# Kernel optimization log

Measured on AMD Instinct MI355X. Metric: run time of the kernel, lower is better.

The kernel has to match this reference:

```python
import jax, jax.numpy as jnp
from jax import lax
import numpy as np

D = 4      # agent_state_vector_length
H = 32     # hidden width (hardcoded in module)
N = 128    # agents
T = 100    # timesteps


def setup_inputs() -> dict:
    key = jax.random.key(0)
    ks = jax.random.split(key, 16)
    g = lambda k, s: jax.random.normal(k, s, dtype=jnp.float32) * 0.05
    return {
        "x": jax.random.normal(ks[0], (N, T, D), dtype=jnp.float32),
        # Conv1d weights stored [out_ch, in_ch, k] (OIH)
        "w1": g(ks[1], (16, D, 3)), "b1": g(ks[2], (16,)),
        "w2": g(ks[3], (32, 16, 3)), "b2": g(ks[4], (32,)),
        "w3": g(ks[5], (32, 32, 3)), "b3": g(ks[6], (32,)),
        # Linear weights stored [in, out]
        "We": g(ks[7], (2 * H, H)), "be": g(ks[8], (H,)),
        "Wa": g(ks[9], (H, H)),     "ba": g(ks[10], (H,)),
        "Wu": g(ks[11], (2 * H, H)), "bu": g(ks[12], (H,)),
        "Wd": g(ks[13], (H, D)),    "bd": g(ks[14], (D,)),
    }


def _forward(x, w1, b1, w2, b2, w3, b3, We, be, Wa, ba, Wu, bu, Wd, bd):
    # ---- conv_1d: per-agent temporal encoder (agents batched) ----
    h = jnp.transpose(x, (0, 2, 1))  # [N, D, T]
    def conv(h, w, b):
        y = lax.conv_general_dilated(h, w, (1,), 'VALID',
                                     dimension_numbers=('NCH', 'OIH', 'NCH'))
        return jax.nn.relu(y + b[None, :, None])
    h = conv(h, w1, b1)
    h = conv(h, w2, b2)
    h = conv(h, w3, b3)            # [N, H, T-6]
    h = jnp.transpose(h, (2, 0, 1))  # [T', N, H]  (time_steps)
    Tp = h.shape[0]

    # ---- graph_conv: all-pairs edge MLP + sum aggregation (j != i) ----
    Wj, Wi = We[:H], We[H:]          # concat(node_j, node_i) split
    ej = jnp.einsum('tjc,cd->tjd', h, Wj)  # sender part
    ei = jnp.einsum('tic,cd->tid', h, Wi)  # receiver part
    e = jax.nn.relu(ej[:, None, :, :] + ei[:, :, None, :] + be)  # [T',i,j,H]
    diag = jax.nn.relu(ej + ei + be)       # i == j terms, excluded by loop
    agg = e.sum(axis=2) - diag             # [T', N, H]
    agg = jax.nn.relu(agg @ Wa + ba)
    upd = jax.nn.relu(h @ Wu[:H] + agg @ Wu[H:] + bu)  # concat(node_i, agg)

    # ---- decode: residual over original state at t+6 ----
    dec = upd @ Wd + bd                    # [T', N, D]
    out = x[:, 6:6 + Tp] + jnp.transpose(dec, (1, 0, 2))  # [N, T', D]
    return out


def reference(x, w1, b1, w2, b2, w3, b3, We, be, Wa, ba, Wu, bu, Wd, bd):
    return _forward(x, w1, b1, w2, b2, w3, b3, We, be, Wa, ba, Wu, bu, Wd, bd)
```

## Files before the change

kernel.cpp:

```cpp
#include <hip/hip_runtime.h>


#define NN 128
#define TT 100
#define TP 94
#define HH 32

__global__ __launch_bounds__(256) void k_conv(
    const float* __restrict__ x,
    const float* __restrict__ w1, const float* __restrict__ b1,
    const float* __restrict__ w2, const float* __restrict__ b2,
    const float* __restrict__ w3, const float* __restrict__ b3,
    const float* __restrict__ We,
    float* __restrict__ h_g, float* __restrict__ ej_g, float* __restrict__ ei_g)
{
    __shared__ float sx[4][72];
    __shared__ float s1[16][68];
    __shared__ float s2[32][64];
    __shared__ float s3[32][48];

    const int n    = blockIdx.x;
    const int half = blockIdx.y;
    const int t0g  = half * 46;
    const int tid  = threadIdx.x;

    if (tid < 72) {
        float4 v = make_float4(0.f, 0.f, 0.f, 0.f);
        if (tid < 54) v = ((const float4*)x)[n * TT + t0g + tid];
        sx[0][tid] = v.x; sx[1][tid] = v.y; sx[2][tid] = v.z; sx[3][tid] = v.w;
    }
    __syncthreads();

    for (int idx = tid; idx < 16 * 68; idx += 256) {
        int o = idx / 68, t = idx - o * 68;
        float acc = b1[o];
        #pragma unroll
        for (int i = 0; i < 4; ++i)
            #pragma unroll
            for (int k = 0; k < 3; ++k)
                acc += sx[i][t + k] * w1[o * 12 + i * 3 + k];
        s1[o][t] = fmaxf(acc, 0.f);
    }
    __syncthreads();

    {
        const int o = tid & 31, seg = tid >> 5;
        const int t0 = seg * 8;
        float acc[8];
        float bv = b2[o];
        #pragma unroll
        for (int u = 0; u < 8; ++u) acc[u] = bv;
        #pragma unroll
        for (int i = 0; i < 16; ++i) {
            float4 f0 = *(const float4*)&s1[i][t0];
            float4 f1 = *(const float4*)&s1[i][t0 + 4];
            float4 f2 = *(const float4*)&s1[i][t0 + 8];
            float a[12] = {f0.x, f0.y, f0.z, f0.w, f1.x, f1.y, f1.z, f1.w,
                           f2.x, f2.y, f2.z, f2.w};
            float W0 = w2[o * 48 + i * 3 + 0];
            float W1 = w2[o * 48 + i * 3 + 1];
            float W2 = w2[o * 48 + i * 3 + 2];
            #pragma unroll
            for (int u = 0; u < 8; ++u)
                acc[u] += a[u] * W0 + a[u + 1] * W1 + a[u + 2] * W2;
        }
        #pragma unroll
        for (int u = 0; u < 8; ++u) s2[o][t0 + u] = fmaxf(acc[u], 0.f);
    }
    __syncthreads();

    {
        const int o = tid & 31, seg = tid >> 5;
        if (seg < 6) {
            const int t0 = seg * 8;
            float acc[8];
            float bv = b3[o];
            #pragma unroll
            for (int u = 0; u < 8; ++u) acc[u] = bv;
            #pragma unroll
            for (int i = 0; i < 32; ++i) {
                float4 f0 = *(const float4*)&s2[i][t0];
                float4 f1 = *(const float4*)&s2[i][t0 + 4];
                float4 f2 = *(const float4*)&s2[i][t0 + 8];
                float a[12] = {f0.x, f0.y, f0.z, f0.w, f1.x, f1.y, f1.z, f1.w,
                               f2.x, f2.y, f2.z, f2.w};
                float W0 = w3[o * 96 + i * 3 + 0];
                float W1 = w3[o * 96 + i * 3 + 1];
                float W2 = w3[o * 96 + i * 3 + 2];
                #pragma unroll
                for (int u = 0; u < 8; ++u)
                    acc[u] += a[u] * W0 + a[u + 1] * W1 + a[u + 2] * W2;
            }
            #pragma unroll
            for (int u = 0; u < 8; ++u) s3[o][t0 + u] = fmaxf(acc[u], 0.f);
        }
    }
    __syncthreads();

    for (int idx = tid; idx < 48 * 32; idx += 256) {
        int tl = idx >> 5, o = idx & 31;
        h_g[((t0g + tl) * NN + n) * HH + o] = s3[o][tl];
    }

    {
        const int d = tid & 31, seg = tid >> 5;
        if (seg < 6) {
            const int t0 = seg * 8;
            float aj[8], ai[8];
            #pragma unroll
            for (int u = 0; u < 8; ++u) { aj[u] = 0.f; ai[u] = 0.f; }
            #pragma unroll
            for (int c = 0; c < 32; ++c) {
                float4 f0 = *(const float4*)&s3[c][t0];
                float4 f1 = *(const float4*)&s3[c][t0 + 4];
                float hv[8] = {f0.x, f0.y, f0.z, f0.w, f1.x, f1.y, f1.z, f1.w};
                float wj = We[c * 32 + d];
                float wi = We[(32 + c) * 32 + d];
                #pragma unroll
                for (int u = 0; u < 8; ++u) {
                    aj[u] += hv[u] * wj;
                    ai[u] += hv[u] * wi;
                }
            }
            #pragma unroll
            for (int u = 0; u < 8; ++u) {
                int tg = t0g + t0 + u;
                ej_g[(tg * NN + n) * HH + d] = aj[u];
                ei_g[(tg * NN + n) * HH + d] = ai[u];
            }
        }
    }
}

__global__ __launch_bounds__(256) void k_agg(
    const float* __restrict__ x,
    const float* __restrict__ h_g, const float* __restrict__ ej_g,
    const float* __restrict__ ei_g,
    const float* __restrict__ be, const float* __restrict__ Wa,
    const float* __restrict__ ba, const float* __restrict__ Wu,
    const float* __restrict__ bu, const float* __restrict__ Wd,
    const float* __restrict__ bd, float* __restrict__ out)
{
    const int t  = blockIdx.x;
    const int ib = blockIdx.y;
    const int tid = threadIdx.x;

    __shared__ float sej[NN * HH];
    __shared__ float sei[32 * HH];
    __shared__ float sh[32 * HH];
    __shared__ float sagg[32 * HH];
    __shared__ float sagg2[32 * HH];
    __shared__ float supd[32 * HH];

    {
        const float4* ej4 = (const float4*)(ej_g + t * NN * HH);
        float4* s4 = (float4*)sej;
        #pragma unroll
        for (int u = 0; u < 4; ++u) s4[tid + 256 * u] = ej4[tid + 256 * u];
        const float4* ei4 = (const float4*)(ei_g + (t * NN + ib * 32) * HH);
        const float4* h4  = (const float4*)(h_g  + (t * NN + ib * 32) * HH);
        ((float4*)sei)[tid] = ei4[tid];
        ((float4*)sh)[tid]  = h4[tid];
    }
    __syncthreads();

    const int d  = tid & 31;
    const int i0 = tid >> 5;

    {
        float bev = be[d];
        float c[4], acc[4];
        #pragma unroll
        for (int u = 0; u < 4; ++u) {
            int i = i0 + u * 8;
            c[u] = sei[i * HH + d] + bev;
            acc[u] = -fmaxf(sej[(ib * 32 + i) * HH + d] + c[u], 0.f);
        }
        #pragma unroll 8
        for (int j = 0; j < NN; ++j) {
            float v = sej[j * HH + d];
            #pragma unroll
            for (int u = 0; u < 4; ++u)
                acc[u] += fmaxf(v + c[u], 0.f);
        }
        #pragma unroll
        for (int u = 0; u < 4; ++u)
            sagg[(i0 + u * 8) * HH + d] = acc[u];
    }
    __syncthreads();

    {
        float acc[4];
        float bav = ba[d];
        #pragma unroll
        for (int u = 0; u < 4; ++u) acc[u] = bav;
        #pragma unroll
        for (int c = 0; c < 32; ++c) {
            float wa = Wa[c * 32 + d];
            #pragma unroll
            for (int u = 0; u < 4; ++u)
                acc[u] += sagg[(i0 + u * 8) * HH + c] * wa;
        }
        #pragma unroll
        for (int u = 0; u < 4; ++u)
            sagg2[(i0 + u * 8) * HH + d] = fmaxf(acc[u], 0.f);
    }
    __syncthreads();

    {
        float acc[4];
        float buv = bu[d];
        #pragma unroll
        for (int u = 0; u < 4; ++u) acc[u] = buv;
        #pragma unroll
        for (int c = 0; c < 32; ++c) {
            float wh = Wu[c * 32 + d];
            float wg = Wu[(32 + c) * 32 + d];
            #pragma unroll
            for (int u = 0; u < 4; ++u) {
                int i = i0 + u * 8;
                acc[u] += sh[i * HH + c] * wh + sagg2[i * HH + c] * wg;
            }
        }
        #pragma unroll
        for (int u = 0; u < 4; ++u)
            supd[(i0 + u * 8) * HH + d] = fmaxf(acc[u], 0.f);
    }
    __syncthreads();

    if (tid < 128) {
        int i = tid >> 2, d4 = tid & 3;
        int n = ib * 32 + i;
        float a = bd[d4];
        #pragma unroll
        for (int c = 0; c < 32; ++c)
            a += supd[i * HH + c] * Wd[c * 4 + d4];
        out[n * (TP * 4) + t * 4 + d4] = x[n * (TT * 4) + (6 + t) * 4 + d4] + a;
    }
}

extern "C" void kernel_launch(void* const* d_in, const int* in_sizes, int n_in,
                              void* d_out, int out_size, void* d_ws, size_t ws_size,
                              hipStream_t stream) {
    const float* x  = (const float*)d_in[0];
    const float* w1 = (const float*)d_in[1];
    const float* b1 = (const float*)d_in[2];
    const float* w2 = (const float*)d_in[3];
    const float* b2 = (const float*)d_in[4];
    const float* w3 = (const float*)d_in[5];
    const float* b3 = (const float*)d_in[6];
    const float* We = (const float*)d_in[7];
    const float* be = (const float*)d_in[8];
    const float* Wa = (const float*)d_in[9];
    const float* ba = (const float*)d_in[10];
    const float* Wu = (const float*)d_in[11];
    const float* bu = (const float*)d_in[12];
    const float* Wd = (const float*)d_in[13];
    const float* bd = (const float*)d_in[14];

    float* ws   = (float*)d_ws;
    float* h_g  = ws;
    float* ej_g = ws + TP * NN * HH;
    float* ei_g = ws + 2 * TP * NN * HH;

    k_conv<<<dim3(NN, 2), 256, 0, stream>>>(x, w1, b1, w2, b2, w3, b3, We,
                                            h_g, ej_g, ei_g);
    k_agg<<<dim3(TP, 4), 256, 0, stream>>>(x, h_g, ej_g, ei_g,
                                           be, Wa, ba, Wu, bu, Wd, bd,
                                           (float*)d_out);
}
```

Measured before the change: 102.8 us.

## Fuse conv and graph-aggregation kernels into one cooperative kernel with grid sync

Merges the two kernel launches into a single cooperative kernel of 384 blocks. The first phase computes the conv stack plus the ej/ei projections on time-thirds, and the second phase runs the per-timestep aggregation, separated by a grid-wide sync. Shared memory for the two phases is overlaid through a union, and the conv stage is re-tiled so each thread computes two output channels. This removes one launch and the inter-kernel gap, at the cost of grid-sync overhead and a cooperative-launch residency requirement.

```diff
diff --git a/kernel.cpp b/kernel.cpp
--- a/kernel.cpp
+++ b/kernel.cpp
@@ -1,4 +1,7 @@
 #include <hip/hip_runtime.h>
+#include <hip/hip_cooperative_groups.h>
+
+namespace cg = cooperative_groups;
 
 
 #define NN 128
@@ -6,236 +9,264 @@
 #define TP 94
 #define HH 32
 
-__global__ __launch_bounds__(256) void k_conv(
+union SharedU {
+    struct {
+        float sx[4][40];
+        float s1[16][44];
+        float s2[32][40];
+        float s3[32][32];
+    } a;
+    struct {
+        float sej[NN * HH];
+        float sei[32 * HH];
+        float sh[32 * HH];
+        float sagg[32 * HH];
+        float sagg2[32 * HH];
+        float supd[32 * HH];
+    } b;
+};
+
+__global__ __launch_bounds__(256, 2) void k_fused(
     const float* __restrict__ x,
     const float* __restrict__ w1, const float* __restrict__ b1,
     const float* __restrict__ w2, const float* __restrict__ b2,
     const float* __restrict__ w3, const float* __restrict__ b3,
-    const float* __restrict__ We,
-    float* __restrict__ h_g, float* __restrict__ ej_g, float* __restrict__ ei_g)
+    const float* __restrict__ We, const float* __restrict__ be,
+    const float* __restrict__ Wa, const float* __restrict__ ba,
+    const float* __restrict__ Wu, const float* __restrict__ bu,
+    const float* __restrict__ Wd, const float* __restrict__ bd,
+    float* __restrict__ h_g, float* __restrict__ ej_g,
+    float* __restrict__ ei_g, float* __restrict__ out)
 {
-    __shared__ float sx[4][72];
-    __shared__ float s1[16][68];
-    __shared__ float s2[32][64];
-    __shared__ float s3[32][48];
-
-    const int n    = blockIdx.x;
-    const int half = blockIdx.y;
-    const int t0g  = half * 46;
-    const int tid  = threadIdx.x;
-
-    if (tid < 72) {
-        float4 v = make_float4(0.f, 0.f, 0.f, 0.f);
-        if (tid < 54) v = ((const float4*)x)[n * TT + t0g + tid];
-        sx[0][tid] = v.x; sx[1][tid] = v.y; sx[2][tid] = v.z; sx[3][tid] = v.w;
+    __shared__ SharedU S;
+    const int tid = threadIdx.x;
+
+    {
+        const int bid   = blockIdx.x;
+        const int n     = bid / 3;
+        const int third = bid - n * 3;
+        const int t0g   = third * 31;
+
+        if (tid < 38) {
+            float4 v = ((const float4*)x)[n * TT + t0g + tid];
+            S.a.sx[0][tid] = v.x; S.a.sx[1][tid] = v.y;
+            S.a.sx[2][tid] = v.z; S.a.sx[3][tid] = v.w;
+        }
+        __syncthreads();
+
+        for (int idx = tid; idx < 16 * 36; idx += 256) {
+            int o = idx / 36, t = idx - o * 36;
+            float acc = b1[o];
+            #pragma unroll
+            for (int i = 0; i < 4; ++i)
+                #pragma unroll
+                for (int k = 0; k < 3; ++k)
+                    acc += S.a.sx[i][t + k] * w1[o * 12 + i * 3 + k];
+            S.a.s1[o][t] = fmaxf(acc, 0.f);
+        }
+        __syncthreads();
+
+        {
+            const int o = tid & 15, seg = tid >> 4;
+            if (seg < 5) {
+                const int t0 = seg * 8;
+                float acc0[8], acc1[8];
+                float bv0 = b2[o], bv1 = b2[o + 16];
+                #pragma unroll
+                for (int u = 0; u < 8; ++u) { acc0[u] = bv0; acc1[u] = bv1; }
+                #pragma unroll
+                for (int i = 0; i < 16; ++i) {
+                    float4 f0 = *(const float4*)&S.a.s1[i][t0];
+                    float4 f1 = *(const float4*)&S.a.s1[i][t0 + 4];
+                    float4 f2 = *(const float4*)&S.a.s1[i][t0 + 8];
+                    float a[12] = {f0.x, f0.y, f0.z, f0.w, f1.x, f1.y, f1.z,
+                                   f1.w, f2.x, f2.y, f2.z, f2.w};
+                    float W00 = w2[o * 48 + i * 3 + 0];
+                    float W01 = w2[o * 48 + i * 3 + 1];
+                    float W02 = w2[o * 48 + i * 3 + 2];
+                    float W10 = w2[(o + 16) * 48 + i * 3 + 0];
+                    float W11 = w2[(o + 16) * 48 + i * 3 + 1];
+                    float W12 = w2[(o + 16) * 48 + i * 3 + 2];
+                    #pragma unroll
+                    for (int u = 0; u < 8; ++u) {
+                        acc0[u] += a[u] * W00 + a[u + 1] * W01 + a[u + 2] * W02;
+                        acc1[u] += a[u] * W10 + a[u + 1] * W11 + a[u + 2] * W12;
+                    }
+                }
+                #pragma unroll
+                for (int u = 0; u < 8; ++u) {
+                    S.a.s2[o][t0 + u]      = fmaxf(acc0[u], 0.f);
+                    S.a.s2[o + 16][t0 + u] = fmaxf(acc1[u], 0.f);
+                }
+            }
+        }
+        __syncthreads();
+
+        {
+            const int o = tid & 15, seg = tid >> 4;
+            if (seg < 4) {
+                const int t0 = seg * 8;
+                float acc0[8], acc1[8];
+                float bv0 = b3[o], bv1 = b3[o + 16];
+                #pragma unroll
+                for (int u = 0; u < 8; ++u) { acc0[u] = bv0; acc1[u] = bv1; }
+                #pragma unroll
+                for (int i = 0; i < 32; ++i) {
+                    float4 f0 = *(const float4*)&S.a.s2[i][t0];
+                    float4 f1 = *(const float4*)&S.a.s2[i][t0 + 4];
+                    float4 f2 = *(const float4*)&S.a.s2[i][t0 + 8];
+                    float a[12] = {f0.x, f0.y, f0.z, f0.w, f1.x, f1.y, f1.z,
+                                   f1.w, f2.x, f2.y, f2.z, f2.w};
+                    float W00 = w3[o * 96 + i * 3 + 0];
+                    float W01 = w3[o * 96 + i * 3 + 1];
+                    float W02 = w3[o * 96 + i * 3 + 2];
+                    float W10 = w3[(o + 16) * 96 + i * 3 + 0];
+                    float W11 = w3[(o + 16) * 96 + i * 3 + 1];
+                    float W12 = w3[(o + 16) * 96 + i * 3 + 2];
+                    #pragma unroll
+                    for (int u = 0; u < 8; ++u) {
+                        acc0[u] += a[u] * W00 + a[u + 1] * W01 + a[u + 2] * W02;
+                        acc1[u] += a[u] * W10 + a[u + 1] * W11 + a[u + 2] * W12;
+                    }
+                }
+                #pragma unroll
+                for (int u = 0; u < 8; ++u) {
+                    S.a.s3[o][t0 + u]      = fmaxf(acc0[u], 0.f);
+                    S.a.s3[o + 16][t0 + u] = fmaxf(acc1[u], 0.f);
+                }
+            }
+        }
+        __syncthreads();
+
+        for (int idx = tid; idx < 32 * 32; idx += 256) {
+            int tl = idx >> 5, o = idx & 31;
+            h_g[((t0g + tl) * NN + n) * HH + o] = S.a.s3[o][tl];
+        }
+
+        {
+            const int d = tid & 31, seg = tid >> 5;
+            if (seg < 4) {
+                const int t0 = seg * 8;
+                float aj[8], ai[8];
+                #pragma unroll
+                for (int u = 0; u < 8; ++u) { aj[u] = 0.f; ai[u] = 0.f; }
+                #pragma unroll
+                for (int c = 0; c < 32; ++c) {
+                    float4 f0 = *(const float4*)&S.a.s3[c][t0];
+                    float4 f1 = *(const float4*)&S.a.s3[c][t0 + 4];
+                    float hv[8] = {f0.x, f0.y, f0.z, f0.w, f1.x, f1.y, f1.z, f1.w};
+                    float wj = We[c * 32 + d];
+                    float wi = We[(32 + c) * 32 + d];
+                    #pragma unroll
+                    for (int u = 0; u < 8; ++u) {
+                        aj[u] += hv[u] * wj;
+                        ai[u] += hv[u] * wi;
+                    }
+                }
+                #pragma unroll
+                for (int u = 0; u < 8; ++u) {
+                    int tg = t0g + t0 + u;
+                    ej_g[(tg * NN + n) * HH + d] = aj[u];
+                    ei_g[(tg * NN + n) * HH + d] = ai[u];
+                }
+            }
+        }
     }
-    __syncthreads();
-
-    for (int idx = tid; idx < 16 * 68; idx += 256) {
-        int o = idx / 68, t = idx - o * 68;
-        float acc = b1[o];
-        #pragma unroll
-        for (int i = 0; i < 4; ++i)
-            #pragma unroll
-            for (int k = 0; k < 3; ++k)
-                acc += sx[i][t + k] * w1[o * 12 + i * 3 + k];
-        s1[o][t] = fmaxf(acc, 0.f);
-    }
-    __syncthreads();
+
+    cg::this_grid().sync();
 
     {
-        const int o = tid & 31, seg = tid >> 5;
-        const int t0 = seg * 8;
-        float acc[8];
-        float bv = b2[o];
-        #pragma unroll
-        for (int u = 0; u < 8; ++u) acc[u] = bv;
-        #pragma unroll
-        for (int i = 0; i < 16; ++i) {
-            float4 f0 = *(const float4*)&s1[i][t0];
-            float4 f1 = *(const float4*)&s1[i][t0 + 4];
-            float4 f2 = *(const float4*)&s1[i][t0 + 8];
-            float a[12] = {f0.x, f0.y, f0.z, f0.w, f1.x, f1.y, f1.z, f1.w,
-                           f2.x, f2.y, f2.z, f2.w};
-            float W0 = w2[o * 48 + i * 3 + 0];
-            float W1 = w2[o * 48 + i * 3 + 1];
-            float W2 = w2[o * 48 + i * 3 + 2];
-            #pragma unroll
-            for (int u = 0; u < 8; ++u)
-                acc[u] += a[u] * W0 + a[u + 1] * W1 + a[u + 2] * W2;
-        }
-        #pragma unroll
-        for (int u = 0; u < 8; ++u) s2[o][t0 + u] = fmaxf(acc[u], 0.f);
-    }
-    __syncthreads();
-
-    {
-        const int o = tid & 31, seg = tid >> 5;
-        if (seg < 6) {
-            const int t0 = seg * 8;
-            float acc[8];
-            float bv = b3[o];
-            #pragma unroll
-            for (int u = 0; u < 8; ++u) acc[u] = bv;
-            #pragma unroll
-            for (int i = 0; i < 32; ++i) {
-                float4 f0 = *(const float4*)&s2[i][t0];
-                float4 f1 = *(const float4*)&s2[i][t0 + 4];
-                float4 f2 = *(const float4*)&s2[i][t0 + 8];
-                float a[12] = {f0.x, f0.y, f0.z, f0.w, f1.x, f1.y, f1.z, f1.w,
-                               f2.x, f2.y, f2.z, f2.w};
-                float W0 = w3[o * 96 + i * 3 + 0];
-                float W1 = w3[o * 96 + i * 3 + 1];
-                float W2 = w3[o * 96 + i * 3 + 2];
-                #pragma unroll
-                for (int u = 0; u < 8; ++u)
-                    acc[u] += a[u] * W0 + a[u + 1] * W1 + a[u + 2] * W2;
-            }
-            #pragma unroll
-            for (int u = 0; u < 8; ++u) s3[o][t0 + u] = fmaxf(acc[u], 0.f);
-        }
-    }
-    __syncthreads();
-
-    for (int idx = tid; idx < 48 * 32; idx += 256) {
-        int tl = idx >> 5, o = idx & 31;
-        h_g[((t0g + tl) * NN + n) * HH + o] = s3[o][tl];
-    }
-
-    {
-        const int d = tid & 31, seg = tid >> 5;
-        if (seg < 6) {
-            const int t0 = seg * 8;
-            float aj[8], ai[8];
-            #pragma unroll
-            for (int u = 0; u < 8; ++u) { aj[u] = 0.f; ai[u] = 0.f; }
-            #pragma unroll
-            for (int c = 0; c < 32; ++c) {
-                float4 f0 = *(const float4*)&s3[c][t0];
-                float4 f1 = *(const float4*)&s3[c][t0 + 4];
-                float hv[8] = {f0.x, f0.y, f0.z, f0.w, f1.x, f1.y, f1.z, f1.w};
-                float wj = We[c * 32 + d];
-                float wi = We[(32 + c) * 32 + d];
-                #pragma unroll
-                for (int u = 0; u < 8; ++u) {
-                    aj[u] += hv[u] * wj;
-                    ai[u] += hv[u] * wi;
-                }
-            }
-            #pragma unroll
-            for (int u = 0; u < 8; ++u) {
-                int tg = t0g + t0 + u;
-                ej_g[(tg * NN + n) * HH + d] = aj[u];
-                ei_g[(tg * NN + n) * HH + d] = ai[u];
-            }
-        }
-    }
-}
-
-__global__ __launch_bounds__(256) void k_agg(
-    const float* __restrict__ x,
-    const float* __restrict__ h_g, const float* __restrict__ ej_g,
-    const float* __restrict__ ei_g,
-    const float* __restrict__ be, const float* __restrict__ Wa,
-    const float* __restrict__ ba, const float* __restrict__ Wu,
-    const float* __restrict__ bu, const float* __restrict__ Wd,
-    const float* __restrict__ bd, float* __restrict__ out)
-{
-    const int t  = blockIdx.x;
-    const int ib = blockIdx.y;
-    const int tid = threadIdx.x;
-
-    __shared__ float sej[NN * HH];
-    __shared__ float sei[32 * HH];
-    __shared__ float sh[32 * HH];
-    __shared__ float sagg[32 * HH];
-    __shared__ float sagg2[32 * HH];
-    __shared__ float supd[32 * HH];
-
-    {
-        const float4* ej4 = (const float4*)(ej_g + t * NN * HH);
-        float4* s4 = (float4*)sej;
-        #pragma unroll
-        for (int u = 0; u < 4; ++u) s4[tid + 256 * u] = ej4[tid + 256 * u];
-        const float4* ei4 = (const float4*)(ei_g + (t * NN + ib * 32) * HH);
-        const float4* h4  = (const float4*)(h_g  + (t * NN + ib * 32) * HH);
-        ((float4*)sei)[tid] = ei4[tid];
-        ((float4*)sh)[tid]  = h4[tid];
-    }
-    __syncthreads();
-
-    const int d  = tid & 31;
-    const int i0 = tid >> 5;
-
-    {
-        float bev = be[d];
-        float c[4], acc[4];
-        #pragma unroll
-        for (int u = 0; u < 4; ++u) {
-            int i = i0 + u * 8;
-            c[u] = sei[i * HH + d] + bev;
-            acc[u] = -fmaxf(sej[(ib * 32 + i) * HH + d] + c[u], 0.f);
-        }
-        #pragma unroll 8
-        for (int j = 0; j < NN; ++j) {
-            float v = sej[j * HH + d];
-            #pragma unroll
-            for (int u = 0; u < 4; ++u)
-                acc[u] += fmaxf(v + c[u], 0.f);
-        }
-        #pragma unroll
-        for (int u = 0; u < 4; ++u)
-            sagg[(i0 + u * 8) * HH + d] = acc[u];
-    }
-    __syncthreads();
-
-    {
-        float acc[4];
-        float bav = ba[d];
-        #pragma unroll
-        for (int u = 0; u < 4; ++u) acc[u] = bav;
-        #pragma unroll
-        for (int c = 0; c < 32; ++c) {
-            float wa = Wa[c * 32 + d];
-            #pragma unroll
-            for (int u = 0; u < 4; ++u)
-                acc[u] += sagg[(i0 + u * 8) * HH + c] * wa;
-        }
-        #pragma unroll
-        for (int u = 0; u < 4; ++u)
-            sagg2[(i0 + u * 8) * HH + d] = fmaxf(acc[u], 0.f);
-    }
-    __syncthreads();
-
-    {
-        float acc[4];
-        float buv = bu[d];
-        #pragma unroll
-        for (int u = 0; u < 4; ++u) acc[u] = buv;
-        #pragma unroll
-        for (int c = 0; c < 32; ++c) {
-            float wh = Wu[c * 32 + d];
-            float wg = Wu[(32 + c) * 32 + d];
-            #pragma unroll
-            for (int u = 0; u < 4; ++u) {
-                int i = i0 + u * 8;
-                acc[u] += sh[i * HH + c] * wh + sagg2[i * HH + c] * wg;
-            }
-        }
-        #pragma unroll
-        for (int u = 0; u < 4; ++u)
-            supd[(i0 + u * 8) * HH + d] = fmaxf(acc[u], 0.f);
-    }
-    __syncthreads();
-
-    if (tid < 128) {
-        int i = tid >> 2, d4 = tid & 3;
-        int n = ib * 32 + i;
-        float a = bd[d4];
-        #pragma unroll
-        for (int c = 0; c < 32; ++c)
-            a += supd[i * HH + c] * Wd[c * 4 + d4];
-        out[n * (TP * 4) + t * 4 + d4] = x[n * (TT * 4) + (6 + t) * 4 + d4] + a;
+        const int tile = blockIdx.x;
+        if (tile < TP * 4) {
+            const int t  = tile >> 2;
+            const int ib = tile & 3;
+
+            {
+                const float4* ej4 = (const float4*)(ej_g + t * NN * HH);
+                float4* s4 = (float4*)S.b.sej;
+                #pragma unroll
+                for (int u = 0; u < 4; ++u) s4[tid + 256 * u] = ej4[tid + 256 * u];
+                const float4* ei4 = (const float4*)(ei_g + (t * NN + ib * 32) * HH);
+                const float4* h4  = (const float4*)(h_g  + (t * NN + ib * 32) * HH);
+                ((float4*)S.b.sei)[tid] = ei4[tid];
+                ((float4*)S.b.sh)[tid]  = h4[tid];
+            }
+            __syncthreads();
+
+            const int d  = tid & 31;
+            const int i0 = tid >> 5;
+
+            {
+                float bev = be[d];
+                float c[4], acc[4];
+                #pragma unroll
+                for (int u = 0; u < 4; ++u) {
+                    int i = i0 + u * 8;
+                    c[u] = S.b.sei[i * HH + d] + bev;
+                    acc[u] = -fmaxf(S.b.sej[(ib * 32 + i) * HH + d] + c[u], 0.f);
+                }
+                #pragma unroll 8
+                for (int j = 0; j < NN; ++j) {
+                    float v = S.b.sej[j * HH + d];
+                    #pragma unroll
+                    for (int u = 0; u < 4; ++u)
+                        acc[u] += fmaxf(v + c[u], 0.f);
+                }
+                #pragma unroll
+                for (int u = 0; u < 4; ++u)
+                    S.b.sagg[(i0 + u * 8) * HH + d] = acc[u];
+            }
+            __syncthreads();
+
+            {
+                float acc[4];
+                float bav = ba[d];
+                #pragma unroll
+                for (int u = 0; u < 4; ++u) acc[u] = bav;
+                #pragma unroll
+                for (int c = 0; c < 32; ++c) {
+                    float wa = Wa[c * 32 + d];
+                    #pragma unroll
+                    for (int u = 0; u < 4; ++u)
+                        acc[u] += S.b.sagg[(i0 + u * 8) * HH + c] * wa;
+                }
+                #pragma unroll
+                for (int u = 0; u < 4; ++u)
+                    S.b.sagg2[(i0 + u * 8) * HH + d] = fmaxf(acc[u], 0.f);
+            }
+            __syncthreads();
+
+            {
+                float acc[4];
+                float buv = bu[d];
+                #pragma unroll
+                for (int u = 0; u < 4; ++u) acc[u] = buv;
+                #pragma unroll
+                for (int c = 0; c < 32; ++c) {
+                    float wh = Wu[c * 32 + d];
+                    float wg = Wu[(32 + c) * 32 + d];
+                    #pragma unroll
+                    for (int u = 0; u < 4; ++u) {
+                        int i = i0 + u * 8;
+                        acc[u] += S.b.sh[i * HH + c] * wh + S.b.sagg2[i * HH + c] * wg;
+                    }
+                }
+                #pragma unroll
+                for (int u = 0; u < 4; ++u)
+                    S.b.supd[(i0 + u * 8) * HH + d] = fmaxf(acc[u], 0.f);
+            }
+            __syncthreads();
+
+            if (tid < 128) {
+                int i = tid >> 2, d4 = tid & 3;
+                int n = ib * 32 + i;
+                float a = bd[d4];
+                #pragma unroll
+                for (int c = 0; c < 32; ++c)
+                    a += S.b.supd[i * HH + c] * Wd[c * 4 + d4];
+                out[n * (TP * 4) + t * 4 + d4] = x[n * (TT * 4) + (6 + t) * 4 + d4] + a;
+            }
+        }
     }
 }
 
@@ -262,10 +293,14 @@
     float* h_g  = ws;
     float* ej_g = ws + TP * NN * HH;
     float* ei_g = ws + 2 * TP * NN * HH;
-
-    k_conv<<<dim3(NN, 2), 256, 0, stream>>>(x, w1, b1, w2, b2, w3, b3, We,
-                                            h_g, ej_g, ei_g);
-    k_agg<<<dim3(TP, 4), 256, 0, stream>>>(x, h_g, ej_g, ei_g,
-                                           be, Wa, ba, Wu, bu, Wd, bd,
-                                           (float*)d_out);
+    float* outp = (float*)d_out;
+
+    void* kargs[] = {
+        (void*)&x,  (void*)&w1, (void*)&b1, (void*)&w2, (void*)&b2,
+        (void*)&w3, (void*)&b3, (void*)&We, (void*)&be, (void*)&Wa,
+        (void*)&ba, (void*)&Wu, (void*)&bu, (void*)&Wd, (void*)&bd,
+        (void*)&h_g, (void*)&ej_g, (void*)&ei_g, (void*)&outp
+    };
+    hipLaunchCooperativeKernel((const void*)k_fused, dim3(NN * 3), dim3(256),
+                               kargs, 0, stream);
 }
```

Measured after the change: 172.6 us. +68.0%, slower.
